# Optimization experiments

Hardware: AMD Instinct MI355X
Metric: run time of the kernel (lower is better)

## Reference

```python
import jax, jax.numpy as jnp
import numpy as np

B, CIN, COUT, H, W = 2, 128, 128, 128, 256
KH, KW = 3, 3
CMID = 32  # COUT // low_factor


def setup_inputs() -> dict:
    key = jax.random.key(0)
    ks = jax.random.split(key, 7)
    x = jax.random.normal(ks[0], (B, CIN, H, W), jnp.float32)
    # torchvision deform_conv2d offset layout: [2*KH*KW, Ho, Wo], (dy, dx) per tap
    offset = jax.random.normal(ks[1], (2 * KH * KW, H, W), jnp.float32)
    weight = jax.random.normal(ks[2], (COUT, CIN, KH, KW), jnp.float32) * 0.05
    bias = jax.random.normal(ks[3], (COUT,), jnp.float32) * 0.01
    down_w = jax.random.normal(ks[4], (CMID, 2 * COUT), jnp.float32) * 0.05
    up_w = jax.random.normal(ks[5], (COUT, CMID), jnp.float32) * 0.05
    scale = jnp.float32(1.0)
    return dict(x=x, offset=offset, weight=weight, bias=bias,
                down_w=down_w, up_w=up_w, scale=scale)


def _deform_conv2d(x, offset, weight, bias):
    # stride=1, padding=1, dilation=1, groups=1 (matches init_conv config)
    Bn, C, Hh, Ww = x.shape
    Co, _, kh, kw = weight.shape
    K = kh * kw
    Ho, Wo = offset.shape[-2:]
    off = offset.reshape(K, 2, Ho, Wo)
    dy, dx = off[:, 0], off[:, 1]                      # [K, Ho, Wo]
    ki, kj = jnp.meshgrid(jnp.arange(kh), jnp.arange(kw), indexing='ij')
    ki = ki.reshape(K).astype(jnp.float32)
    kj = kj.reshape(K).astype(jnp.float32)
    i = jnp.arange(Ho, dtype=jnp.float32)
    j = jnp.arange(Wo, dtype=jnp.float32)
    PAD = 1.0
    py = i[None, :, None] - PAD + ki[:, None, None] + dy   # [K, Ho, Wo]
    px = j[None, None, :] - PAD + kj[:, None, None] + dx
    y0 = jnp.floor(py).astype(jnp.int32)
    x0 = jnp.floor(px).astype(jnp.int32)
    fy = py - y0.astype(py.dtype)
    fx = px - x0.astype(px.dtype)
    xf = x.reshape(Bn, C, Hh * Ww)

    def gather(yi, xi, w):
        # zero padding outside the image (torchvision semantics)
        valid = (yi >= 0) & (yi < Hh) & (xi >= 0) & (xi < Ww)
        yc = jnp.clip(yi, 0, Hh - 1)
        xc = jnp.clip(xi, 0, Ww - 1)
        idx = (yc * Ww + xc).reshape(-1)                   # [K*Ho*Wo]
        g = xf[:, :, idx].reshape(Bn, C, K, Ho, Wo)
        return g * (w * valid.astype(w.dtype))[None, None]

    val = gather(y0, x0, (1.0 - fy) * (1.0 - fx))
    val = val + gather(y0, x0 + 1, (1.0 - fy) * fx)
    val = val + gather(y0 + 1, x0, fy * (1.0 - fx))
    val = val + gather(y0 + 1, x0 + 1, fy * fx)
    out = jnp.einsum('bcnij,ocn->boij', val, weight.reshape(Co, C, K))
    return out + bias[None, :, None, None]


def reference(x, offset, weight, bias, down_w, up_w, scale):
    # h = original frozen conv (weights shared with the deform branch, ablation != wo_copy)
    h = jax.lax.conv_general_dilated(
        x, weight, window_strides=(1, 1), padding=[(1, 1), (1, 1)],
        dimension_numbers=('NCHW', 'OIHW', 'NCHW'))
    h = h + bias[None, :, None, None]
    dx = _deform_conv2d(x, offset, weight, bias)
    dx = jnp.concatenate([dx, h], axis=1)                  # mix == 'cat'
    lo = jnp.einsum('bcij,dc->bdij', dx, down_w)           # 1x1 conv_down
    up = jnp.einsum('bcij,dc->bdij', lo, up_w)             # 1x1 conv_up
    return h + scale * up
```

## Files before the change

### kernel.cpp

```cpp
#include <hip/hip_runtime.h>
#include <hip/hip_bf16.h>

typedef __attribute__((ext_vector_type(8))) short short8;
typedef __attribute__((ext_vector_type(8))) unsigned short ushort8;
typedef __attribute__((ext_vector_type(4))) float f32x4;
typedef __attribute__((ext_vector_type(4))) int int4v;
typedef __attribute__((ext_vector_type(4))) float float4v;
typedef __attribute__((ext_vector_type(2))) float float2v;
typedef __attribute__((ext_vector_type(4))) unsigned int uint4v;

#define HH 128
#define WW 256
#define CIN_ 128
#define COUT_ 128

__device__ __forceinline__ float bf2f(unsigned short u) {
  return __builtin_bit_cast(float, ((unsigned int)u) << 16);
}
__device__ __forceinline__ unsigned short f2bf(float f) {
  union { __hip_bfloat16 h; unsigned short u; } v;
  v.h = __float2bfloat16(f);
  return v.u;
}

__global__ void k_prep_T(const float* __restrict__ down_w,
                         const float* __restrict__ weight,
                         float* __restrict__ T) {
  int e = blockIdx.x * 256 + threadIdx.x;
  if (e >= 2 * 32 * 1152) return;
  int s = e / 36864, r = e % 36864, d = r / 1152, ck = r % 1152;
  float a = 0.f;
  #pragma unroll 4
  for (int p = 0; p < 128; ++p)
    a += down_w[d * 256 + s * 128 + p] * weight[p * 1152 + ck];
  T[e] = a;
}

__global__ void k_prep_W(const float* __restrict__ up_w,
                         const float* __restrict__ weight,
                         const float* __restrict__ T,
                         const float* __restrict__ scale,
                         unsigned short* __restrict__ wdef,
                         unsigned short* __restrict__ wstd) {
  int e = blockIdx.x * 256 + threadIdx.x;
  if (e >= 2 * 9 * 128 * 128) return;
  int s = e / 147456, r = e % 147456;
  int tap = r / 16384, o = (r / 128) % 128, c = r % 128;
  int ck = c * 9 + tap;
  const float* Ts = T + s * 36864;
  float a = 0.f;
  #pragma unroll
  for (int d = 0; d < 32; ++d) a += up_w[o * 32 + d] * Ts[d * 1152 + ck];
  float scl = scale[0];
  int idx = ((tap * 4 + (c >> 5)) * 128 + o) * 32 + (c & 31);
  if (s == 1) {
    wstd[idx] = f2bf(weight[o * 1152 + ck] + scl * a);
  } else {
    wdef[idx] = f2bf(scl * a);
  }
}

__global__ void k_prep_bias(const float* __restrict__ down_w,
                            const float* __restrict__ up_w,
                            const float* __restrict__ bias,
                            const float* __restrict__ scale,
                            float* __restrict__ beff) {
  __shared__ float sd[32];
  int t = threadIdx.x;
  if (t < 32) {
    float a = 0.f;
    for (int p = 0; p < 128; ++p)
      a += (down_w[t * 256 + p] + down_w[t * 256 + 128 + p]) * bias[p];
    sd[t] = a;
  }
  __syncthreads();
  if (t < 128) {
    float a = 0.f;
    #pragma unroll
    for (int d = 0; d < 32; ++d) a += up_w[t * 32 + d] * sd[d];
    beff[t] = bias[t] + scale[0] * a;
  }
}

__global__ __launch_bounds__(256) void k_nhwc(const float* __restrict__ x,
                                              unsigned short* __restrict__ xh) {
  __shared__ float tile[32 * 129];
  int idx = blockIdx.x;
  int b = idx >> 10, rem = idx & 1023;
  int y = rem >> 3, xg = (rem & 7) << 5;
  int tid = threadIdx.x;
  for (int it = tid; it < 32 * 128; it += 256) {
    int c = it >> 5, xi = it & 31;
    tile[xi * 129 + c] = x[(((size_t)b * 128 + c) * 128 + y) * 256 + xg + xi];
  }
  __syncthreads();
  for (int it = tid; it < 32 * 16; it += 256) {
    int xi = it >> 4, cs = it & 15;
    ushort8 v;
    #pragma unroll
    for (int e = 0; e < 8; ++e) v[e] = f2bf(tile[xi * 129 + cs * 8 + e]);
    *(ushort8*)(xh + (((size_t)b * 128 + y) * 256 + xg + xi) * 128 + cs * 8) = v;
  }
}

__global__ void k_meta(const float* __restrict__ offset,
                       int4v* __restrict__ mo, float4v* __restrict__ mw) {
  int e = blockIdx.x * 256 + threadIdx.x;
  if (e >= 9 * 128 * 256) return;
  int k = e >> 15, rem = e & 32767;
  int ii = rem >> 8, jj = rem & 255;
  float dy = offset[(2 * k) * 32768 + rem];
  float dx = offset[(2 * k + 1) * 32768 + rem];
  int ki = k / 3, kj = k % 3;
  float py = (float)(ii - 1 + ki) + dy;
  float px = (float)(jj - 1 + kj) + dx;
  float fy0 = floorf(py), fx0 = floorf(px);
  int y0 = (int)fy0, x0 = (int)fx0;
  float fy = py - fy0, fx = px - fx0;
  int ys[2] = {y0, y0 + 1};
  int xs_[2] = {x0, x0 + 1};
  float wy[2] = {1.f - fy, fy}, wx[2] = {1.f - fx, fx};
  int4v o;
  float4v w;
  #pragma unroll
  for (int cy = 0; cy < 2; ++cy) {
    #pragma unroll
    for (int cx = 0; cx < 2; ++cx) {
      int yy = ys[cy], xx = xs_[cx];
      bool valid = (yy >= 0) && (yy < HH) && (xx < WW) && (xx >= 0);
      int yc = min(max(yy, 0), HH - 1), xc = min(max(xx, 0), WW - 1);
      int off = (yc * WW + xc) * CIN_;
      float wv = valid ? wy[cy] * wx[cx] : 0.f;
      int ci = cy * 2 + cx;
      if (ci == 0) { o.x = off; w.x = wv; }
      else if (ci == 1) { o.y = off; w.y = wv; }
      else if (ci == 2) { o.z = off; w.z = wv; }
      else { o.w = off; w.w = wv; }
    }
  }
  mo[e] = o;
  mw[e] = w;
}

__global__ __launch_bounds__(512, 4) void k_main(
    const unsigned short* __restrict__ xh,
    const int4v* __restrict__ mo, const float4v* __restrict__ mw,
    const unsigned short* __restrict__ wstd, const unsigned short* __restrict__ wdef,
    const float* __restrict__ beff, float* __restrict__ out) {
  __shared__ __align__(16) unsigned short sbuf[2][128 * 128];

  int orig = blockIdx.x;
  int t = ((orig & 7) << 6) + (orig >> 3);
  int b = t >> 8, i = (t >> 1) & 127, j0 = (t & 1) << 7;
  int tid = threadIdx.x;
  const unsigned short* xb = xh + (size_t)b * (HH * WW * CIN_);

  int slot = tid & 15, pg = tid >> 4;
  int ce = slot * 8;

  int lane = tid & 63, wid = tid >> 6;
  int obase = (wid >> 1) << 5;
  int pixbase = (wid & 1) << 6;
  int lrow = lane & 15, lhi = lane >> 4;

  f32x4 acc[2][4] = {};

  auto COMB = [&](uint4v* g, float4v w, int q, unsigned short* buf) {
    int p = q * 32 + pg;
    uint4v r;
    #pragma unroll
    for (int wi = 0; wi < 4; ++wi) {
      unsigned u0 = g[0][wi], u1 = g[1][wi], u2 = g[2][wi], u3 = g[3][wi];
      float2v f0 = {__builtin_bit_cast(float, u0 << 16), __builtin_bit_cast(float, u0 & 0xffff0000u)};
      float2v f1 = {__builtin_bit_cast(float, u1 << 16), __builtin_bit_cast(float, u1 & 0xffff0000u)};
      float2v f2 = {__builtin_bit_cast(float, u2 << 16), __builtin_bit_cast(float, u2 & 0xffff0000u)};
      float2v f3 = {__builtin_bit_cast(float, u3 << 16), __builtin_bit_cast(float, u3 & 0xffff0000u)};
      float2v s = w.x * f0 + w.y * f1 + w.z * f2 + w.w * f3;
      unsigned rr;
      asm("v_cvt_pk_bf16_f32 %0, %1, %2" : "=v"(rr) : "v"(s.x), "v"(s.y));
      r[wi] = rr;
    }
    *(uint4v*)((char*)buf + (p << 8) + ((slot ^ (p & 15)) << 4)) = r;
  };

  auto STAGE_DEF = [&](int tap, unsigned short* buf) {
    int4v o;
    float4v wq0, wq1;
    uint4v g0[4], g1[4];
    int mbase = (tap * HH + i) * WW + j0 + pg;

    o = mo[mbase]; wq0 = mw[mbase];
    g0[0] = *(const uint4v*)(xb + o.x + ce);
    g0[1] = *(const uint4v*)(xb + o.y + ce);
    g0[2] = *(const uint4v*)(xb + o.z + ce);
    g0[3] = *(const uint4v*)(xb + o.w + ce);
    o = mo[mbase + 32]; wq1 = mw[mbase + 32];
    g1[0] = *(const uint4v*)(xb + o.x + ce);
    g1[1] = *(const uint4v*)(xb + o.y + ce);
    g1[2] = *(const uint4v*)(xb + o.z + ce);
    g1[3] = *(const uint4v*)(xb + o.w + ce);

    COMB(g0, wq0, 0, buf);
    o = mo[mbase + 64]; wq0 = mw[mbase + 64];
    g0[0] = *(const uint4v*)(xb + o.x + ce);
    g0[1] = *(const uint4v*)(xb + o.y + ce);
    g0[2] = *(const uint4v*)(xb + o.z + ce);
    g0[3] = *(const uint4v*)(xb + o.w + ce);
    COMB(g1, wq1, 1, buf);
    o = mo[mbase + 96]; wq1 = mw[mbase + 96];
    g1[0] = *(const uint4v*)(xb + o.x + ce);
    g1[1] = *(const uint4v*)(xb + o.y + ce);
    g1[2] = *(const uint4v*)(xb + o.z + ce);
    g1[3] = *(const uint4v*)(xb + o.w + ce);
    COMB(g0, wq0, 2, buf);
    COMB(g1, wq1, 3, buf);
  };

  auto STAGE_STD = [&](int tap, unsigned short* buf) {
    int ki = tap / 3, kj = tap % 3;
    int gy = i - 1 + ki;
    bool oky = (unsigned)gy < (unsigned)HH;
    uint4v s[4];
    #pragma unroll
    for (int q = 0; q < 4; ++q) {
      int p = q * 32 + pg;
      int gx = j0 + p - 1 + kj;
      uint4v vv = {};
      if (oky && (unsigned)gx < (unsigned)WW)
        vv = *(const uint4v*)(xb + (size_t)(gy * WW + gx) * CIN_ + ce);
      s[q] = vv;
    }
    #pragma unroll
    for (int q = 0; q < 4; ++q) {
      int p = q * 32 + pg;
      *(uint4v*)((char*)buf + (p << 8) + ((slot ^ (p & 15)) << 4)) = s[q];
    }
  };

  auto COMPUTE = [&](int v) {
    const unsigned short* cur = sbuf[v & 1];
    const unsigned short* wt = ((v & 1) ? wdef : wstd) + (size_t)(v >> 1) * 16384;
    short8 af[4][2];
    #pragma unroll
    for (int cc = 0; cc < 4; ++cc)
      #pragma unroll
      for (int am = 0; am < 2; ++am)
        af[cc][am] = *(const short8*)(wt + ((size_t)(cc * 128 + obase + am * 16 + lrow)) * 32 + lhi * 8);
    #pragma unroll
    for (int cc = 0; cc < 4; ++cc) {
      short8 bfr[4];
      #pragma unroll
      for (int bn = 0; bn < 4; ++bn) {
        int pp = pixbase + bn * 16 + lrow;
        bfr[bn] = *(const short8*)((const char*)cur + (pp << 8) +
                                   (((cc * 4 + lhi) ^ lrow) << 4));
      }
      #pragma unroll
      for (int am = 0; am < 2; ++am)
        #pragma unroll
        for (int bn = 0; bn < 4; ++bn)
          acc[am][bn] = __builtin_amdgcn_mfma_f32_16x16x32_bf16(af[cc][am], bfr[bn], acc[am][bn], 0, 0, 0);
    }
  };

  STAGE_STD(0, sbuf[0]);
  __syncthreads();

  for (int v = 0; v < 18; ++v) {
    if (v < 17) {
      int nv = v + 1;
      if (nv & 1) STAGE_DEF(nv >> 1, sbuf[nv & 1]);
      else        STAGE_STD(nv >> 1, sbuf[nv & 1]);
    }
    COMPUTE(v);
    __syncthreads();
  }

  #pragma unroll
  for (int am = 0; am < 2; ++am) {
    #pragma unroll
    for (int bn = 0; bn < 4; ++bn) {
      int jg = j0 + pixbase + bn * 16 + lrow;
      #pragma unroll
      for (int r = 0; r < 4; ++r) {
        int o = obase + am * 16 + lhi * 4 + r;
        out[(((size_t)b * COUT_ + o) * HH + i) * WW + jg] = acc[am][bn][r] + beff[o];
      }
    }
  }
}

extern "C" void kernel_launch(void* const* d_in, const int* in_sizes, int n_in,
                              void* d_out, int out_size, void* d_ws, size_t ws_size,
                              hipStream_t stream) {
  const float* x      = (const float*)d_in[0];
  const float* offset = (const float*)d_in[1];
  const float* weight = (const float*)d_in[2];
  const float* bias   = (const float*)d_in[3];
  const float* down_w = (const float*)d_in[4];
  const float* up_w   = (const float*)d_in[5];
  const float* scale  = (const float*)d_in[6];
  float* out = (float*)d_out;

  char* ws = (char*)d_ws;
  unsigned short* xh   = (unsigned short*)(ws);
  int4v* mo            = (int4v*)(ws + 16777216);
  float4v* mw          = (float4v*)(ws + 21495808);
  unsigned short* wstd = (unsigned short*)(ws + 26214400);
  unsigned short* wdef = (unsigned short*)(ws + 26509312);
  float* T             = (float*)(ws + 26804224);
  float* beff          = (float*)(ws + 27099136);

  k_prep_T<<<dim3(288), dim3(256), 0, stream>>>(down_w, weight, T);
  k_prep_W<<<dim3(1152), dim3(256), 0, stream>>>(up_w, weight, T, scale, wdef, wstd);
  k_prep_bias<<<dim3(1), dim3(128), 0, stream>>>(down_w, up_w, bias, scale, beff);
  k_nhwc<<<dim3(2048), dim3(256), 0, stream>>>(x, xh);
  k_meta<<<dim3(1152), dim3(256), 0, stream>>>(offset, mo, mw);
  k_main<<<dim3(512), dim3(512), 0, stream>>>(xh, mo, mw, wstd, wdef, beff, out);
}
```

Measured before the change: 115.6 us.

## Warp-specialize main kernel into producer/consumer halves and merge prep kernels

The main kernel now runs 1024 threads per block: 512 threads only gather and stage input tiles into shared memory while a separate 512 threads only run the MFMA loop, with both sides stepping through matching barrier counts. The aim is to overlap the gather latency with matrix compute without making one thread do both. Four small prep kernels are also folded into one multi-role launch to cut launch overhead. In exchange, each block doubles its thread count, which lowers occupancy, and the design depends on both halves issuing exactly the same number of __syncthreads calls.

```diff
diff --git a/kernel.cpp b/kernel.cpp
--- a/kernel.cpp
+++ b/kernel.cpp
@@ -14,18 +14,15 @@
 #define CIN_ 128
 #define COUT_ 128
 
-__device__ __forceinline__ float bf2f(unsigned short u) {
-  return __builtin_bit_cast(float, ((unsigned int)u) << 16);
-}
 __device__ __forceinline__ unsigned short f2bf(float f) {
   union { __hip_bfloat16 h; unsigned short u; } v;
   v.h = __float2bfloat16(f);
   return v.u;
 }
 
-__global__ void k_prep_T(const float* __restrict__ down_w,
-                         const float* __restrict__ weight,
-                         float* __restrict__ T) {
+__global__ __launch_bounds__(256) void k_pre1(
+    const float* __restrict__ down_w, const float* __restrict__ weight,
+    float* __restrict__ T) {
   int e = blockIdx.x * 256 + threadIdx.x;
   if (e >= 2 * 32 * 1152) return;
   int s = e / 36864, r = e % 36864, d = r / 1152, ck = r % 1152;
@@ -36,113 +33,104 @@
   T[e] = a;
 }
 
-__global__ void k_prep_W(const float* __restrict__ up_w,
-                         const float* __restrict__ weight,
-                         const float* __restrict__ T,
-                         const float* __restrict__ scale,
-                         unsigned short* __restrict__ wdef,
-                         unsigned short* __restrict__ wstd) {
-  int e = blockIdx.x * 256 + threadIdx.x;
-  if (e >= 2 * 9 * 128 * 128) return;
-  int s = e / 147456, r = e % 147456;
-  int tap = r / 16384, o = (r / 128) % 128, c = r % 128;
-  int ck = c * 9 + tap;
-  const float* Ts = T + s * 36864;
-  float a = 0.f;
-  #pragma unroll
-  for (int d = 0; d < 32; ++d) a += up_w[o * 32 + d] * Ts[d * 1152 + ck];
-  float scl = scale[0];
-  int idx = ((tap * 4 + (c >> 5)) * 128 + o) * 32 + (c & 31);
-  if (s == 1) {
-    wstd[idx] = f2bf(weight[o * 1152 + ck] + scl * a);
-  } else {
-    wdef[idx] = f2bf(scl * a);
-  }
-}
-
-__global__ void k_prep_bias(const float* __restrict__ down_w,
-                            const float* __restrict__ up_w,
-                            const float* __restrict__ bias,
-                            const float* __restrict__ scale,
-                            float* __restrict__ beff) {
-  __shared__ float sd[32];
-  int t = threadIdx.x;
-  if (t < 32) {
-    float a = 0.f;
-    for (int p = 0; p < 128; ++p)
-      a += (down_w[t * 256 + p] + down_w[t * 256 + 128 + p]) * bias[p];
-    sd[t] = a;
-  }
-  __syncthreads();
-  if (t < 128) {
+__global__ __launch_bounds__(256) void k_pre2(
+    const float* __restrict__ x, unsigned short* __restrict__ xh,
+    const float* __restrict__ offset, int4v* __restrict__ mo,
+    float4v* __restrict__ mw,
+    const float* __restrict__ up_w, const float* __restrict__ weight,
+    const float* __restrict__ T, const float* __restrict__ scale,
+    unsigned short* __restrict__ wdef, unsigned short* __restrict__ wstd,
+    const float* __restrict__ down_w, const float* __restrict__ bias,
+    float* __restrict__ beff) {
+  __shared__ float tile[32 * 129];
+  int bid = blockIdx.x;
+  int tid = threadIdx.x;
+
+  if (bid < 2048) {
+    int idx = bid;
+    int b = idx >> 10, rem = idx & 1023;
+    int y = rem >> 3, xg = (rem & 7) << 5;
+    for (int it = tid; it < 32 * 128; it += 256) {
+      int c = it >> 5, xi = it & 31;
+      tile[xi * 129 + c] = x[(((size_t)b * 128 + c) * 128 + y) * 256 + xg + xi];
+    }
+    __syncthreads();
+    for (int it = tid; it < 32 * 16; it += 256) {
+      int xi = it >> 4, cs = it & 15;
+      ushort8 v;
+      #pragma unroll
+      for (int e = 0; e < 8; ++e) v[e] = f2bf(tile[xi * 129 + cs * 8 + e]);
+      *(ushort8*)(xh + (((size_t)b * 128 + y) * 256 + xg + xi) * 128 + cs * 8) = v;
+    }
+  } else if (bid < 3200) {
+    int e = (bid - 2048) * 256 + tid;
+    int k = e >> 15, rem = e & 32767;
+    int ii = rem >> 8, jj = rem & 255;
+    float dy = offset[(2 * k) * 32768 + rem];
+    float dx = offset[(2 * k + 1) * 32768 + rem];
+    int ki = k / 3, kj = k % 3;
+    float py = (float)(ii - 1 + ki) + dy;
+    float px = (float)(jj - 1 + kj) + dx;
+    float fy0 = floorf(py), fx0 = floorf(px);
+    int y0 = (int)fy0, x0 = (int)fx0;
+    float fy = py - fy0, fx = px - fx0;
+    int ys[2] = {y0, y0 + 1};
+    int xs_[2] = {x0, x0 + 1};
+    float wy[2] = {1.f - fy, fy}, wx[2] = {1.f - fx, fx};
+    int4v o;
+    float4v w;
+    #pragma unroll
+    for (int cy = 0; cy < 2; ++cy) {
+      #pragma unroll
+      for (int cx = 0; cx < 2; ++cx) {
+        int yy = ys[cy], xx = xs_[cx];
+        bool valid = (yy >= 0) && (yy < HH) && (xx < WW) && (xx >= 0);
+        int yc = min(max(yy, 0), HH - 1), xc = min(max(xx, 0), WW - 1);
+        int off = (yc * WW + xc) * CIN_;
+        float wv = valid ? wy[cy] * wx[cx] : 0.f;
+        int ci = cy * 2 + cx;
+        if (ci == 0) { o.x = off; w.x = wv; }
+        else if (ci == 1) { o.y = off; w.y = wv; }
+        else if (ci == 2) { o.z = off; w.z = wv; }
+        else { o.w = off; w.w = wv; }
+      }
+    }
+    mo[e] = o;
+    mw[e] = w;
+  } else if (bid < 4352) {
+    int e = (bid - 3200) * 256 + tid;
+    int s = e / 147456, r = e % 147456;
+    int tap = r / 16384, o = (r / 128) % 128, c = r % 128;
+    int ck = c * 9 + tap;
+    const float* Ts = T + s * 36864;
     float a = 0.f;
     #pragma unroll
-    for (int d = 0; d < 32; ++d) a += up_w[t * 32 + d] * sd[d];
-    beff[t] = bias[t] + scale[0] * a;
+    for (int d = 0; d < 32; ++d) a += up_w[o * 32 + d] * Ts[d * 1152 + ck];
+    float scl = scale[0];
+    int idx = ((tap * 4 + (c >> 5)) * 128 + o) * 32 + (c & 31);
+    if (s == 1) {
+      wstd[idx] = f2bf(weight[o * 1152 + ck] + scl * a);
+    } else {
+      wdef[idx] = f2bf(scl * a);
+    }
+  } else {
+    if (tid < 32) {
+      float a = 0.f;
+      for (int p = 0; p < 128; ++p)
+        a += (down_w[tid * 256 + p] + down_w[tid * 256 + 128 + p]) * bias[p];
+      tile[tid] = a;
+    }
+    __syncthreads();
+    if (tid < 128) {
+      float a = 0.f;
+      #pragma unroll
+      for (int d = 0; d < 32; ++d) a += up_w[tid * 32 + d] * tile[d];
+      beff[tid] = bias[tid] + scale[0] * a;
+    }
   }
 }
 
-__global__ __launch_bounds__(256) void k_nhwc(const float* __restrict__ x,
-                                              unsigned short* __restrict__ xh) {
-  __shared__ float tile[32 * 129];
-  int idx = blockIdx.x;
-  int b = idx >> 10, rem = idx & 1023;
-  int y = rem >> 3, xg = (rem & 7) << 5;
-  int tid = threadIdx.x;
-  for (int it = tid; it < 32 * 128; it += 256) {
-    int c = it >> 5, xi = it & 31;
-    tile[xi * 129 + c] = x[(((size_t)b * 128 + c) * 128 + y) * 256 + xg + xi];
-  }
-  __syncthreads();
-  for (int it = tid; it < 32 * 16; it += 256) {
-    int xi = it >> 4, cs = it & 15;
-    ushort8 v;
-    #pragma unroll
-    for (int e = 0; e < 8; ++e) v[e] = f2bf(tile[xi * 129 + cs * 8 + e]);
-    *(ushort8*)(xh + (((size_t)b * 128 + y) * 256 + xg + xi) * 128 + cs * 8) = v;
-  }
-}
-
-__global__ void k_meta(const float* __restrict__ offset,
-                       int4v* __restrict__ mo, float4v* __restrict__ mw) {
-  int e = blockIdx.x * 256 + threadIdx.x;
-  if (e >= 9 * 128 * 256) return;
-  int k = e >> 15, rem = e & 32767;
-  int ii = rem >> 8, jj = rem & 255;
-  float dy = offset[(2 * k) * 32768 + rem];
-  float dx = offset[(2 * k + 1) * 32768 + rem];
-  int ki = k / 3, kj = k % 3;
-  float py = (float)(ii - 1 + ki) + dy;
-  float px = (float)(jj - 1 + kj) + dx;
-  float fy0 = floorf(py), fx0 = floorf(px);
-  int y0 = (int)fy0, x0 = (int)fx0;
-  float fy = py - fy0, fx = px - fx0;
-  int ys[2] = {y0, y0 + 1};
-  int xs_[2] = {x0, x0 + 1};
-  float wy[2] = {1.f - fy, fy}, wx[2] = {1.f - fx, fx};
-  int4v o;
-  float4v w;
-  #pragma unroll
-  for (int cy = 0; cy < 2; ++cy) {
-    #pragma unroll
-    for (int cx = 0; cx < 2; ++cx) {
-      int yy = ys[cy], xx = xs_[cx];
-      bool valid = (yy >= 0) && (yy < HH) && (xx < WW) && (xx >= 0);
-      int yc = min(max(yy, 0), HH - 1), xc = min(max(xx, 0), WW - 1);
-      int off = (yc * WW + xc) * CIN_;
-      float wv = valid ? wy[cy] * wx[cx] : 0.f;
-      int ci = cy * 2 + cx;
-      if (ci == 0) { o.x = off; w.x = wv; }
-      else if (ci == 1) { o.y = off; w.y = wv; }
-      else if (ci == 2) { o.z = off; w.z = wv; }
-      else { o.w = off; w.w = wv; }
-    }
-  }
-  mo[e] = o;
-  mw[e] = w;
-}
-
-__global__ __launch_bounds__(512, 4) void k_main(
+__global__ __launch_bounds__(1024, 8) void k_main(
     const unsigned short* __restrict__ xh,
     const int4v* __restrict__ mo, const float4v* __restrict__ mw,
     const unsigned short* __restrict__ wstd, const unsigned short* __restrict__ wdef,
@@ -155,136 +143,141 @@
   int tid = threadIdx.x;
   const unsigned short* xb = xh + (size_t)b * (HH * WW * CIN_);
 
-  int slot = tid & 15, pg = tid >> 4;
-  int ce = slot * 8;
-
-  int lane = tid & 63, wid = tid >> 6;
-  int obase = (wid >> 1) << 5;
-  int pixbase = (wid & 1) << 6;
-  int lrow = lane & 15, lhi = lane >> 4;
-
-  f32x4 acc[2][4] = {};
-
-  auto COMB = [&](uint4v* g, float4v w, int q, unsigned short* buf) {
-    int p = q * 32 + pg;
-    uint4v r;
+  bool producer = tid < 512;
+
+  if (producer) {
+    int slot = tid & 15, pg = tid >> 4;
+    int ce = slot * 8;
+
+    auto COMB = [&](uint4v* g, float4v w, int q, unsigned short* buf) {
+      int p = q * 32 + pg;
+      uint4v r;
+      #pragma unroll
+      for (int wi = 0; wi < 4; ++wi) {
+        unsigned u0 = g[0][wi], u1 = g[1][wi], u2 = g[2][wi], u3 = g[3][wi];
+        float2v f0 = {__builtin_bit_cast(float, u0 << 16), __builtin_bit_cast(float, u0 & 0xffff0000u)};
+        float2v f1 = {__builtin_bit_cast(float, u1 << 16), __builtin_bit_cast(float, u1 & 0xffff0000u)};
+        float2v f2 = {__builtin_bit_cast(float, u2 << 16), __builtin_bit_cast(float, u2 & 0xffff0000u)};
+        float2v f3 = {__builtin_bit_cast(float, u3 << 16), __builtin_bit_cast(float, u3 & 0xffff0000u)};
+        float2v s = w.x * f0 + w.y * f1 + w.z * f2 + w.w * f3;
+        unsigned rr;
+        asm("v_cvt_pk_bf16_f32 %0, %1, %2" : "=v"(rr) : "v"(s.x), "v"(s.y));
+        r[wi] = rr;
+      }
+      *(uint4v*)((char*)buf + (p << 8) + ((slot ^ (p & 15)) << 4)) = r;
+    };
+
+    auto STAGE_DEF = [&](int tap, unsigned short* buf) {
+      int4v o;
+      float4v wq0, wq1;
+      uint4v g0[4], g1[4];
+      int mbase = (tap * HH + i) * WW + j0 + pg;
+
+      o = mo[mbase]; wq0 = mw[mbase];
+      g0[0] = *(const uint4v*)(xb + o.x + ce);
+      g0[1] = *(const uint4v*)(xb + o.y + ce);
+      g0[2] = *(const uint4v*)(xb + o.z + ce);
+      g0[3] = *(const uint4v*)(xb + o.w + ce);
+      o = mo[mbase + 32]; wq1 = mw[mbase + 32];
+      g1[0] = *(const uint4v*)(xb + o.x + ce);
+      g1[1] = *(const uint4v*)(xb + o.y + ce);
+      g1[2] = *(const uint4v*)(xb + o.z + ce);
+      g1[3] = *(const uint4v*)(xb + o.w + ce);
+
+      COMB(g0, wq0, 0, buf);
+      o = mo[mbase + 64]; wq0 = mw[mbase + 64];
+      g0[0] = *(const uint4v*)(xb + o.x + ce);
+      g0[1] = *(const uint4v*)(xb + o.y + ce);
+      g0[2] = *(const uint4v*)(xb + o.z + ce);
+      g0[3] = *(const uint4v*)(xb + o.w + ce);
+      COMB(g1, wq1, 1, buf);
+      o = mo[mbase + 96]; wq1 = mw[mbase + 96];
+      g1[0] = *(const uint4v*)(xb + o.x + ce);
+      g1[1] = *(const uint4v*)(xb + o.y + ce);
+      g1[2] = *(const uint4v*)(xb + o.z + ce);
+      g1[3] = *(const uint4v*)(xb + o.w + ce);
+      COMB(g0, wq0, 2, buf);
+      COMB(g1, wq1, 3, buf);
+    };
+
+    auto STAGE_STD = [&](int tap, unsigned short* buf) {
+      int ki = tap / 3, kj = tap % 3;
+      int gy = i - 1 + ki;
+      bool oky = (unsigned)gy < (unsigned)HH;
+      uint4v s[4];
+      #pragma unroll
+      for (int q = 0; q < 4; ++q) {
+        int p = q * 32 + pg;
+        int gx = j0 + p - 1 + kj;
+        uint4v vv = {};
+        if (oky && (unsigned)gx < (unsigned)WW)
+          vv = *(const uint4v*)(xb + (size_t)(gy * WW + gx) * CIN_ + ce);
+        s[q] = vv;
+      }
+      #pragma unroll
+      for (int q = 0; q < 4; ++q) {
+        int p = q * 32 + pg;
+        *(uint4v*)((char*)buf + (p << 8) + ((slot ^ (p & 15)) << 4)) = s[q];
+      }
+    };
+
+    STAGE_STD(0, sbuf[0]);
+    __syncthreads();
+    for (int v = 0; v < 18; ++v) {
+      if (v < 17) {
+        int nv = v + 1;
+        if (nv & 1) STAGE_DEF(nv >> 1, sbuf[nv & 1]);
+        else        STAGE_STD(nv >> 1, sbuf[nv & 1]);
+      }
+      __syncthreads();
+    }
+  } else {
+    int ctid = tid - 512;
+    int lane = ctid & 63, wid = ctid >> 6;
+    int obase = (wid >> 1) << 5;
+    int pixbase = (wid & 1) << 6;
+    int lrow = lane & 15, lhi = lane >> 4;
+
+    f32x4 acc[2][4] = {};
+
+    __syncthreads();
+    for (int v = 0; v < 18; ++v) {
+      const unsigned short* cur = sbuf[v & 1];
+      const unsigned short* wt = ((v & 1) ? wdef : wstd) + (size_t)(v >> 1) * 16384;
+      short8 af[4][2];
+      #pragma unroll
+      for (int cc = 0; cc < 4; ++cc)
+        #pragma unroll
+        for (int am = 0; am < 2; ++am)
+          af[cc][am] = *(const short8*)(wt + ((size_t)(cc * 128 + obase + am * 16 + lrow)) * 32 + lhi * 8);
+      #pragma unroll
+      for (int cc = 0; cc < 4; ++cc) {
+        short8 bfr[4];
+        #pragma unroll
+        for (int bn = 0; bn < 4; ++bn) {
+          int pp = pixbase + bn * 16 + lrow;
+          bfr[bn] = *(const short8*)((const char*)cur + (pp << 8) +
+                                     (((cc * 4 + lhi) ^ lrow) << 4));
+        }
+        #pragma unroll
+        for (int am = 0; am < 2; ++am)
+          #pragma unroll
+          for (int bn = 0; bn < 4; ++bn)
+            acc[am][bn] = __builtin_amdgcn_mfma_f32_16x16x32_bf16(af[cc][am], bfr[bn], acc[am][bn], 0, 0, 0);
+      }
+      __syncthreads();
+    }
+
     #pragma unroll
-    for (int wi = 0; wi < 4; ++wi) {
-      unsigned u0 = g[0][wi], u1 = g[1][wi], u2 = g[2][wi], u3 = g[3][wi];
-      float2v f0 = {__builtin_bit_cast(float, u0 << 16), __builtin_bit_cast(float, u0 & 0xffff0000u)};
-      float2v f1 = {__builtin_bit_cast(float, u1 << 16), __builtin_bit_cast(float, u1 & 0xffff0000u)};
-      float2v f2 = {__builtin_bit_cast(float, u2 << 16), __builtin_bit_cast(float, u2 & 0xffff0000u)};
-      float2v f3 = {__builtin_bit_cast(float, u3 << 16), __builtin_bit_cast(float, u3 & 0xffff0000u)};
-      float2v s = w.x * f0 + w.y * f1 + w.z * f2 + w.w * f3;
-      unsigned rr;
-      asm("v_cvt_pk_bf16_f32 %0, %1, %2" : "=v"(rr) : "v"(s.x), "v"(s.y));
-      r[wi] = rr;
-    }
-    *(uint4v*)((char*)buf + (p << 8) + ((slot ^ (p & 15)) << 4)) = r;
-  };
-
-  auto STAGE_DEF = [&](int tap, unsigned short* buf) {
-    int4v o;
-    float4v wq0, wq1;
-    uint4v g0[4], g1[4];
-    int mbase = (tap * HH + i) * WW + j0 + pg;
-
-    o = mo[mbase]; wq0 = mw[mbase];
-    g0[0] = *(const uint4v*)(xb + o.x + ce);
-    g0[1] = *(const uint4v*)(xb + o.y + ce);
-    g0[2] = *(const uint4v*)(xb + o.z + ce);
-    g0[3] = *(const uint4v*)(xb + o.w + ce);
-    o = mo[mbase + 32]; wq1 = mw[mbase + 32];
-    g1[0] = *(const uint4v*)(xb + o.x + ce);
-    g1[1] = *(const uint4v*)(xb + o.y + ce);
-    g1[2] = *(const uint4v*)(xb + o.z + ce);
-    g1[3] = *(const uint4v*)(xb + o.w + ce);
-
-    COMB(g0, wq0, 0, buf);
-    o = mo[mbase + 64]; wq0 = mw[mbase + 64];
-    g0[0] = *(const uint4v*)(xb + o.x + ce);
-    g0[1] = *(const uint4v*)(xb + o.y + ce);
-    g0[2] = *(const uint4v*)(xb + o.z + ce);
-    g0[3] = *(const uint4v*)(xb + o.w + ce);
-    COMB(g1, wq1, 1, buf);
-    o = mo[mbase + 96]; wq1 = mw[mbase + 96];
-    g1[0] = *(const uint4v*)(xb + o.x + ce);
-    g1[1] = *(const uint4v*)(xb + o.y + ce);
-    g1[2] = *(const uint4v*)(xb + o.z + ce);
-    g1[3] = *(const uint4v*)(xb + o.w + ce);
-    COMB(g0, wq0, 2, buf);
-    COMB(g1, wq1, 3, buf);
-  };
-
-  auto STAGE_STD = [&](int tap, unsigned short* buf) {
-    int ki = tap / 3, kj = tap % 3;
-    int gy = i - 1 + ki;
-    bool oky = (unsigned)gy < (unsigned)HH;
-    uint4v s[4];
-    #pragma unroll
-    for (int q = 0; q < 4; ++q) {
-      int p = q * 32 + pg;
-      int gx = j0 + p - 1 + kj;
-      uint4v vv = {};
-      if (oky && (unsigned)gx < (unsigned)WW)
-        vv = *(const uint4v*)(xb + (size_t)(gy * WW + gx) * CIN_ + ce);
-      s[q] = vv;
-    }
-    #pragma unroll
-    for (int q = 0; q < 4; ++q) {
-      int p = q * 32 + pg;
-      *(uint4v*)((char*)buf + (p << 8) + ((slot ^ (p & 15)) << 4)) = s[q];
-    }
-  };
-
-  auto COMPUTE = [&](int v) {
-    const unsigned short* cur = sbuf[v & 1];
-    const unsigned short* wt = ((v & 1) ? wdef : wstd) + (size_t)(v >> 1) * 16384;
-    short8 af[4][2];
-    #pragma unroll
-    for (int cc = 0; cc < 4; ++cc)
-      #pragma unroll
-      for (int am = 0; am < 2; ++am)
-        af[cc][am] = *(const short8*)(wt + ((size_t)(cc * 128 + obase + am * 16 + lrow)) * 32 + lhi * 8);
-    #pragma unroll
-    for (int cc = 0; cc < 4; ++cc) {
-      short8 bfr[4];
+    for (int am = 0; am < 2; ++am) {
       #pragma unroll
       for (int bn = 0; bn < 4; ++bn) {
-        int pp = pixbase + bn * 16 + lrow;
-        bfr[bn] = *(const short8*)((const char*)cur + (pp << 8) +
-                                   (((cc * 4 + lhi) ^ lrow) << 4));
-      }
-      #pragma unroll
-      for (int am = 0; am < 2; ++am)
+        int jg = j0 + pixbase + bn * 16 + lrow;
         #pragma unroll
-        for (int bn = 0; bn < 4; ++bn)
-          acc[am][bn] = __builtin_amdgcn_mfma_f32_16x16x32_bf16(af[cc][am], bfr[bn], acc[am][bn], 0, 0, 0);
-    }
-  };
-
-  STAGE_STD(0, sbuf[0]);
-  __syncthreads();
-
-  for (int v = 0; v < 18; ++v) {
-    if (v < 17) {
-      int nv = v + 1;
-      if (nv & 1) STAGE_DEF(nv >> 1, sbuf[nv & 1]);
-      else        STAGE_STD(nv >> 1, sbuf[nv & 1]);
-    }
-    COMPUTE(v);
-    __syncthreads();
-  }
-
-  #pragma unroll
-  for (int am = 0; am < 2; ++am) {
-    #pragma unroll
-    for (int bn = 0; bn < 4; ++bn) {
-      int jg = j0 + pixbase + bn * 16 + lrow;
-      #pragma unroll
-      for (int r = 0; r < 4; ++r) {
-        int o = obase + am * 16 + lhi * 4 + r;
-        out[(((size_t)b * COUT_ + o) * HH + i) * WW + jg] = acc[am][bn][r] + beff[o];
+        for (int r = 0; r < 4; ++r) {
+          int o = obase + am * 16 + lhi * 4 + r;
+          out[(((size_t)b * COUT_ + o) * HH + i) * WW + jg] = acc[am][bn][r] + beff[o];
+        }
       }
     }
   }
@@ -311,10 +304,9 @@
   float* T             = (float*)(ws + 26804224);
   float* beff          = (float*)(ws + 27099136);
 
-  k_prep_T<<<dim3(288), dim3(256), 0, stream>>>(down_w, weight, T);
-  k_prep_W<<<dim3(1152), dim3(256), 0, stream>>>(up_w, weight, T, scale, wdef, wstd);
-  k_prep_bias<<<dim3(1), dim3(128), 0, stream>>>(down_w, up_w, bias, scale, beff);
-  k_nhwc<<<dim3(2048), dim3(256), 0, stream>>>(x, xh);
-  k_meta<<<dim3(1152), dim3(256), 0, stream>>>(offset, mo, mw);
-  k_main<<<dim3(512), dim3(512), 0, stream>>>(xh, mo, mw, wstd, wdef, beff, out);
-}
+  k_pre1<<<dim3(288), dim3(256), 0, stream>>>(down_w, weight, T);
+  k_pre2<<<dim3(4353), dim3(256), 0, stream>>>(x, xh, offset, mo, mw,
+                                               up_w, weight, T, scale,
+                                               wdef, wstd, down_w, bias, beff);
+  k_main<<<dim3(512), dim3(1024), 0, stream>>>(xh, mo, mw, wstd, wdef, beff, out);
+}
```

New measurement: 151.5 us. 31.1% more time.
